# Kernel tuning notes

Measured on AMD Instinct MI355X. Metric: run time of the kernel, lower is better.

## Reference

```python
import jax, jax.numpy as jnp
import numpy as np
import math

H = 16  # n_head
DK = 64  # d_k = n_feat // n_head
BASE = 10000.0


def _rope_cos_sin(T, dk, dtype):
    inv_freq = 1.0 / (BASE ** (jnp.arange(0, dk, 2, dtype=jnp.float32) / dk))
    t = jnp.arange(T, dtype=jnp.float32)
    freqs = jnp.einsum('i,j->ij', t, inv_freq)          # [T, dk/2]
    emb = jnp.concatenate([freqs, freqs], axis=-1)       # [T, dk]
    return jnp.cos(emb).astype(dtype)[:, None, None, :], jnp.sin(emb).astype(dtype)[:, None, None, :]


def _rotate_half(x):
    x1, x2 = jnp.split(x, 2, axis=-1)
    return jnp.concatenate([-x2, x1], axis=-1)


def setup_inputs() -> dict:
    key = jax.random.key(0)
    ks = jax.random.split(key, 8)
    T, B, C = 2048, 2, 1024
    s = 0.02
    return {
        'query': jax.random.normal(ks[0], (T, B, C), jnp.float32),
        'key': jax.random.normal(ks[1], (T, B, C), jnp.float32),
        'value': jax.random.normal(ks[2], (T, B, C), jnp.float32),
        'Wq': jax.random.normal(ks[3], (C, C), jnp.float32) * s,
        'bq': jnp.zeros((C,), jnp.float32),
        'Wk': jax.random.normal(ks[4], (C, C), jnp.float32) * s,
        'bk': jnp.zeros((C,), jnp.float32),
        'Wv': jax.random.normal(ks[5], (C, C), jnp.float32) * s,
        'bv': jnp.zeros((C,), jnp.float32),
        'Wo': jax.random.normal(ks[6], (C, C), jnp.float32) * s,
        'bo': jnp.zeros((C,), jnp.float32),
    }


def reference(query, key, value, Wq, bq, Wk, bk, Wv, bv, Wo, bo):
    T, B, C = value.shape
    # --- RoPE applied to raw inputs (per the original module), before projections ---
    q = query.reshape(T, B, H, DK)
    k = key.reshape(T, B, H, DK)
    cos, sin = _rope_cos_sin(T, DK, q.dtype)  # [T,1,1,DK]
    q = q * cos + _rotate_half(q) * sin
    k = k * cos + _rotate_half(k) * sin
    q = q.reshape(T, B, C).transpose(1, 0, 2)   # [B,T,C]
    k = k.reshape(T, B, C).transpose(1, 0, 2)
    v = value.transpose(1, 0, 2)
    # --- QKV projections (torch Linear: x @ W.T + b) ---
    q = (jnp.einsum('btc,dc->btd', q, Wq) + bq).reshape(B, T, H, DK).transpose(0, 2, 1, 3)
    k = (jnp.einsum('btc,dc->btd', k, Wk) + bk).reshape(B, T, H, DK).transpose(0, 2, 1, 3)
    v = (jnp.einsum('btc,dc->btd', v, Wv) + bv).reshape(B, T, H, DK).transpose(0, 2, 1, 3)
    # --- scaled dot-product attention ---
    scores = jnp.einsum('bhqd,bhkd->bhqk', q, k) / math.sqrt(DK)
    attn = jax.nn.softmax(scores, axis=-1)
    x = jnp.einsum('bhqk,bhkd->bhqd', attn, v)        # [B,H,T,DK]
    x = x.transpose(0, 2, 1, 3).reshape(B, T, C)
    out = jnp.einsum('btc,dc->btd', x, Wo) + bo        # [B,T,C]
    return out.transpose(1, 0, 2)                      # [T,B,C]
```

## Files before the change

kernel.cpp:

```cpp
#include <hip/hip_runtime.h>
#include <hip/hip_bf16.h>
#include <math.h>

#define T_SEQ 2048
#define B_SZ 2
#define C_DIM 1024
#define H_HEADS 16
#define DKH 64
#define M_ROWS (T_SEQ * B_SZ)

#define QSCALE 0.1803368801111204f

typedef __attribute__((ext_vector_type(8))) short bf16x8;
typedef __attribute__((ext_vector_type(4))) float f32x4;
typedef unsigned short ushort_t;


__device__ __forceinline__ ushort_t f2bf(float f) {
    unsigned u = __float_as_uint(f);
    u += 0x7fffu + ((u >> 16) & 1u);
    return (ushort_t)(u >> 16);
}

__device__ __forceinline__ unsigned pack2bf(float a, float b) {
#if __has_builtin(__builtin_amdgcn_cvt_pk_bf16_f32)
    typedef __attribute__((ext_vector_type(2))) __bf16 bf16x2_t;
    union { bf16x2_t v; unsigned u; } cv;
    cv.v = __builtin_amdgcn_cvt_pk_bf16_f32(a, b);
    return cv.u;
#else
    return (unsigned)f2bf(a) | ((unsigned)f2bf(b) << 16);
#endif
}

__device__ __forceinline__ void async_copy16(const void* g, void* l) {
    __builtin_amdgcn_global_load_lds(
        (const __attribute__((address_space(1))) void*)g,
        (__attribute__((address_space(3))) void*)l, 16, 0, 0);
}

__global__ __launch_bounds__(256) void rope_cast_qk(
        const float* __restrict__ q, const float* __restrict__ k,
        ushort_t* __restrict__ qb, ushort_t* __restrict__ kb) {
    int idx  = blockIdx.x * 256 + threadIdx.x;
    int j    = idx & 31;
    int rest = idx >> 5;
    int h    = rest & (H_HEADS - 1);
    int tb   = rest >> 4;
    int t    = tb >> 1;
    float inv = exp2f(-(float)j * 0.41524101186092034f);
    float ang = (float)t * inv;
    float s, c;
    sincosf(ang, &s, &c);
    int base = tb * C_DIM + h * DKH + j;
    float q1 = q[base], q2 = q[base + 32];
    float k1 = k[base], k2 = k[base + 32];
    qb[base]      = f2bf(q1 * c - q2 * s);
    qb[base + 32] = f2bf(q2 * c + q1 * s);
    kb[base]      = f2bf(k1 * c - k2 * s);
    kb[base + 32] = f2bf(k2 * c + k1 * s);
}

__global__ __launch_bounds__(256) void cast_bf16_w4(
        const float* __restrict__ w0, const float* __restrict__ w1,
        const float* __restrict__ w2, const float* __restrict__ w3,
        ushort_t* __restrict__ o0, ushort_t* __restrict__ o1,
        ushort_t* __restrict__ o2, ushort_t* __restrict__ o3) {
    int which = blockIdx.y;
    const float* in = which == 0 ? w0 : which == 1 ? w1 : which == 2 ? w2 : w3;
    ushort_t*   out = which == 0 ? o0 : which == 1 ? o1 : which == 2 ? o2 : o3;
    int i = blockIdx.x * 256 + threadIdx.x;
    float4 v = reinterpret_cast<const float4*>(in)[i];
    ushort4 o;
    o.x = f2bf(v.x); o.y = f2bf(v.y); o.z = f2bf(v.z); o.w = f2bf(v.w);
    reinterpret_cast<ushort4*>(out)[i] = o;
}

__global__ __launch_bounds__(256) void cast_value_perm(
        const float* __restrict__ in, ushort_t* __restrict__ out) {
    int i   = blockIdx.x * 256 + threadIdx.x;
    int c4  = i & 255;
    int row = i >> 8;
    int b   = row >> 11, t = row & 2047;
    float4 v = reinterpret_cast<const float4*>(in)[(t * 2 + b) * 256 + c4];
    ushort4 o;
    o.x = f2bf(v.x); o.y = f2bf(v.y); o.z = f2bf(v.z); o.w = f2bf(v.w);
    reinterpret_cast<ushort4*>(out)[i] = o;
}

template <bool BF16_OUT, bool BIAS_ROW>
__global__ __launch_bounds__(512) void gemm_nt(
        const ushort_t* __restrict__ A, const ushort_t* __restrict__ W,
        const float* __restrict__ bias, void* __restrict__ Cout,
        int M, int N, int K, float scale) {
    __shared__ ushort_t As[2][128 * 64];
    __shared__ ushort_t Bs[2][64 * 64];
    const int tid  = threadIdx.x;
    const int lane = tid & 63;
    const int w    = tid >> 6;
    const int m16  = lane & 15, quad = lane >> 4;
    const int r8   = lane >> 3, c8 = lane & 7;
    const int clog = c8 ^ r8;
    const int rowBase = blockIdx.y * 128;
    const int colBase = blockIdx.x * 64;

    f32x4 acc[4];
#pragma unroll
    for (int j = 0; j < 4; j++) acc[j] = (f32x4){0.f, 0.f, 0.f, 0.f};

    auto stage = [&](int buf, int kt) {
#pragma unroll
        for (int i = 0; i < 2; ++i) {
            int R = w * 16 + i * 8;
            async_copy16(A + (size_t)(rowBase + R + r8) * K + kt + clog * 8,
                         &As[buf][R * 64]);
        }
        {
            int R = w * 8;
            async_copy16(W + (size_t)(colBase + R + r8) * K + kt + clog * 8,
                         &Bs[buf][R * 64]);
        }
    };

    stage(0, 0);
    int cur = 0;
    for (int kt = 0; kt < K; kt += 64, cur ^= 1) {
        if (kt + 64 < K) {
            stage(cur ^ 1, kt + 64);
            asm volatile("s_waitcnt vmcnt(3)" ::: "memory");
        } else {
            asm volatile("s_waitcnt vmcnt(0)" ::: "memory");
        }
        __builtin_amdgcn_s_barrier();
        __builtin_amdgcn_sched_barrier(0);
        const ushort_t* Asc = As[cur];
        const ushort_t* Bsc = Bs[cur];
#pragma unroll
        for (int ks = 0; ks < 2; ++ks) {
            int lc = ks * 4 + quad;
            bf16x8 af;
            {
                int R = w * 16 + m16;
                af = *reinterpret_cast<const bf16x8*>(
                    &Asc[R * 64 + ((lc ^ (R & 7)) << 3)]);
            }
            bf16x8 bfr[4];
#pragma unroll
            for (int ni = 0; ni < 4; ni++) {
                int R = ni * 16 + m16;
                bfr[ni] = *reinterpret_cast<const bf16x8*>(
                    &Bsc[R * 64 + ((lc ^ (R & 7)) << 3)]);
            }
#pragma unroll
            for (int ni = 0; ni < 4; ni++)
                acc[ni] = __builtin_amdgcn_mfma_f32_16x16x32_bf16(
                    af, bfr[ni], acc[ni], 0, 0, 0);
        }
        __builtin_amdgcn_s_barrier();
    }
#pragma unroll
    for (int ni = 0; ni < 4; ni++)
#pragma unroll
        for (int r = 0; r < 4; r++) {
            int row = rowBase + w * 16 + quad * 4 + r;
            int col = colBase + ni * 16 + m16;
            float v = (acc[ni][r] + (BIAS_ROW ? bias[row] : bias[col])) * scale;
            if (BF16_OUT)
                ((ushort_t*)Cout)[(size_t)row * N + col] = f2bf(v);
            else
                ((float*)Cout)[(size_t)row * N + col] = v;
        }
}

__global__ __launch_bounds__(256) void attn(
        const ushort_t* __restrict__ Qp, const ushort_t* __restrict__ Kp,
        const ushort_t* __restrict__ VTg, ushort_t* __restrict__ X) {
    __shared__ char smem[40960];
    ushort_t* Qt = (ushort_t*)smem;
    char*  KtC   = smem + 8192;
    char*  VTC   = smem + 24576;
    float* exch  = (float*)(smem + 8192);
    float* lbuf  = (float*)smem;

    const int tid  = threadIdx.x;
    const int lane = tid & 63;
    const int w    = tid >> 6;
    const int m16  = lane & 15, quad = lane >> 4;
    const int r8   = lane >> 3, c8 = lane & 7;
    const int clog = c8 ^ r8;

    const int lid   = blockIdx.x + blockIdx.y * 32;
    const int jj    = lid >> 3;
    const int pair  = (lid & 7) * 4 + (jj >> 5);
    const int qBase = (jj & 31) * 64;
    const int b = pair >> 4, h = pair & 15;

    const int ofA = m16 * 128 + ((quad ^ (m16 & 7)) << 4);
    const int ofB = m16 * 128 + (((4 + quad) ^ (m16 & 7)) << 4);
    const int sw4 = (m16 >> 1) & 3;
    const int fro = m16 * 64 + ((quad ^ sw4) << 4);
    int pw0[2];
#pragma unroll
    for (int kt_i = 0; kt_i < 2; kt_i++)
        pw0[kt_i] = m16 * 64 + (((kt_i * 2 + (quad >> 1)) ^ sw4) << 4) + (quad & 1) * 8;
    char* PwC = KtC + w * 4096;

    const int vlc = (lane & 3) ^ ((lane >> 3) & 3);

#pragma unroll
    for (int i = 0; i < 2; ++i) {
        int R = w * 16 + i * 8;
        async_copy16(Qp + (size_t)((qBase + R + r8) * 2 + b) * C_DIM + h * DKH + clog * 8,
                     &Qt[R * 64]);
    }
    __syncthreads();
    bf16x8 aq[4][2];
#pragma unroll
    for (int ni = 0; ni < 4; ni++) {
        aq[ni][0] = *reinterpret_cast<const bf16x8*>((const char*)Qt + ni * 2048 + ofA);
        aq[ni][1] = *reinterpret_cast<const bf16x8*>((const char*)Qt + ni * 2048 + ofB);
    }
    asm volatile("s_waitcnt lgkmcnt(0)" ::: "memory");
    __syncthreads();

    float lrun[4] = {0.f, 0.f, 0.f, 0.f};
    f32x4 o[4][4];
#pragma unroll
    for (int mi = 0; mi < 4; mi++)
#pragma unroll
        for (int ni = 0; ni < 4; ni++) o[mi][ni] = (f32x4){0.f, 0.f, 0.f, 0.f};

    auto stageKV = [&](int kt) {
#pragma unroll
        for (int i = 0; i < 4; ++i) {
            int key = kt + w * 32 + i * 8 + r8;
            async_copy16(Kp + (size_t)(key * 2 + b) * C_DIM + h * DKH + clog * 8,
                         KtC + w * 4096 + i * 1024);
        }
#pragma unroll
        for (int i = 0; i < 4; ++i) {
            int dkr = i * 16 + (lane >> 2);
            async_copy16(VTg + (size_t)(h * DKH + dkr) * M_ROWS + b * T_SEQ + kt + w * 32 + vlc * 8,
                         VTC + w * 4096 + i * 1024);
        }
    };

    stageKV(0);
    for (int kt = 0; kt < T_SEQ; kt += 128) {
        asm volatile("s_waitcnt vmcnt(4)" ::: "memory");
        __builtin_amdgcn_sched_barrier(0);

        f32x4 s[2][4];
#pragma unroll
        for (int kt_i = 0; kt_i < 2; kt_i++) {
#pragma unroll
            for (int ni = 0; ni < 4; ni++) s[kt_i][ni] = (f32x4){0.f, 0.f, 0.f, 0.f};
            bf16x8 kf0 = *reinterpret_cast<const bf16x8*>(KtC + w * 4096 + kt_i * 2048 + ofA);
            bf16x8 kf1 = *reinterpret_cast<const bf16x8*>(KtC + w * 4096 + kt_i * 2048 + ofB);
#pragma unroll
            for (int ni = 0; ni < 4; ni++) {
                s[kt_i][ni] = __builtin_amdgcn_mfma_f32_16x16x32_bf16(kf0, aq[ni][0], s[kt_i][ni], 0, 0, 0);
                s[kt_i][ni] = __builtin_amdgcn_mfma_f32_16x16x32_bf16(kf1, aq[ni][1], s[kt_i][ni], 0, 0, 0);
            }
        }

#pragma unroll
        for (int kt_i = 0; kt_i < 2; kt_i++)
#pragma unroll
            for (int ni = 0; ni < 4; ni++) {
                float p0 = __builtin_amdgcn_exp2f(s[kt_i][ni][0]);
                float p1 = __builtin_amdgcn_exp2f(s[kt_i][ni][1]);
                float p2 = __builtin_amdgcn_exp2f(s[kt_i][ni][2]);
                float p3 = __builtin_amdgcn_exp2f(s[kt_i][ni][3]);
                lrun[ni] += (p0 + p1) + (p2 + p3);
                uint2 pv;
                pv.x = pack2bf(p0, p1);
                pv.y = pack2bf(p2, p3);
                *reinterpret_cast<uint2*>(PwC + ni * 1024 + pw0[kt_i]) = pv;
            }
        asm volatile("s_waitcnt lgkmcnt(0)" ::: "memory");

        bf16x8 pf[4];
#pragma unroll
        for (int ni = 0; ni < 4; ni++)
            pf[ni] = *reinterpret_cast<const bf16x8*>(PwC + ni * 1024 + fro);
        asm volatile("s_waitcnt vmcnt(0)" ::: "memory");
        __builtin_amdgcn_sched_barrier(0);
        bf16x8 vfr[4];
#pragma unroll
        for (int mi = 0; mi < 4; mi++)
            vfr[mi] = *reinterpret_cast<const bf16x8*>(VTC + w * 4096 + mi * 1024 + fro);
        asm volatile("s_waitcnt lgkmcnt(0)" ::: "memory");
        __builtin_amdgcn_sched_barrier(0);
        if (kt + 128 < T_SEQ) stageKV(kt + 128);
        __builtin_amdgcn_sched_barrier(0);

#pragma unroll
        for (int mi = 0; mi < 4; mi++)
#pragma unroll
            for (int ni = 0; ni < 4; ni++)
                o[mi][ni] = __builtin_amdgcn_mfma_f32_16x16x32_bf16(vfr[mi], pf[ni], o[mi][ni], 0, 0, 0);
    }

#pragma unroll
    for (int ni = 0; ni < 4; ni++) {
        lrun[ni] += __shfl_xor(lrun[ni], 16);
        lrun[ni] += __shfl_xor(lrun[ni], 32);
    }
    float lv = quad == 0 ? lrun[0] : quad == 1 ? lrun[1] : quad == 2 ? lrun[2] : lrun[3];
    lbuf[w * 64 + quad * 16 + m16] = lv;

    __syncthreads();

#pragma unroll
    for (int rnd = 0; rnd < 2; rnd++) {
        if (rnd) __syncthreads();
#pragma unroll
        for (int t2 = 0; t2 < 2; t2++) {
            int mi = 2 * rnd + t2;
#pragma unroll
            for (int ni = 0; ni < 4; ni++) {
                int q = ni * 16 + m16;
                int cw = t2 * 4 + quad;
                *reinterpret_cast<f32x4*>(
                    &exch[w * 2048 + q * 32 + ((cw ^ (q & 7)) << 2)]) = o[mi][ni];
            }
        }
        __syncthreads();
        int q = tid >> 2;
        float lsum = lbuf[q] + lbuf[64 + q] + lbuf[128 + q] + lbuf[192 + q];
        float invl = 1.0f / lsum;
#pragma unroll
        for (int half = 0; half < 2; half++) {
            int c = (tid & 3) + 4 * half;
            int off = q * 32 + (((c ^ (q & 7))) << 2);
            f32x4 v = *reinterpret_cast<const f32x4*>(&exch[off]);
            f32x4 v1 = *reinterpret_cast<const f32x4*>(&exch[2048 + off]);
            f32x4 v2 = *reinterpret_cast<const f32x4*>(&exch[4096 + off]);
            f32x4 v3 = *reinterpret_cast<const f32x4*>(&exch[6144 + off]);
            v = v + v1 + v2 + v3;
            uint2 pk;
            pk.x = pack2bf(v[0] * invl, v[1] * invl);
            pk.y = pack2bf(v[2] * invl, v[3] * invl);
            int t = qBase + q;
            *reinterpret_cast<uint2*>(
                &X[(size_t)(t * 2 + b) * C_DIM + h * DKH + rnd * 32 + c * 4]) = pk;
        }
    }
}

extern "C" void kernel_launch(void* const* d_in, const int* in_sizes, int n_in,
                              void* d_out, int out_size, void* d_ws, size_t ws_size,
                              hipStream_t stream) {
    const float* query = (const float*)d_in[0];
    const float* key   = (const float*)d_in[1];
    const float* value = (const float*)d_in[2];
    const float* Wq = (const float*)d_in[3];
    const float* bq = (const float*)d_in[4];
    const float* Wk = (const float*)d_in[5];
    const float* bk = (const float*)d_in[6];
    const float* Wv = (const float*)d_in[7];
    const float* bv = (const float*)d_in[8];
    const float* Wo = (const float*)d_in[9];
    const float* bo = (const float*)d_in[10];
    float* out = (float*)d_out;

    ushort_t* qb  = (ushort_t*)d_ws;
    ushort_t* kb  = qb  + (size_t)M_ROWS * C_DIM;
    ushort_t* vb2 = kb  + (size_t)M_ROWS * C_DIM;
    ushort_t* Wqb = vb2 + (size_t)M_ROWS * C_DIM;
    ushort_t* Wkb = Wqb + (size_t)C_DIM * C_DIM;
    ushort_t* Wvb = Wkb + (size_t)C_DIM * C_DIM;
    ushort_t* Wob = Wvb + (size_t)C_DIM * C_DIM;
    ushort_t* Qp  = Wob + (size_t)C_DIM * C_DIM;
    ushort_t* Kp  = Qp  + (size_t)M_ROWS * C_DIM;
    ushort_t* VTg = Kp  + (size_t)M_ROWS * C_DIM;
    ushort_t* Xb  = VTg + (size_t)M_ROWS * C_DIM;

    rope_cast_qk<<<(T_SEQ * B_SZ * H_HEADS * 32) / 256, 256, 0, stream>>>(query, key, qb, kb);
    cast_value_perm<<<(M_ROWS * C_DIM / 4) / 256, 256, 0, stream>>>(value, vb2);
    dim3 cg((C_DIM * C_DIM / 4) / 256, 4);
    cast_bf16_w4<<<cg, 256, 0, stream>>>(Wq, Wk, Wv, Wo, Wqb, Wkb, Wvb, Wob);

    dim3 gg(C_DIM / 64, M_ROWS / 128);
    gemm_nt<true, false><<<gg, 512, 0, stream>>>(qb, Wqb, bq, Qp, M_ROWS, C_DIM, C_DIM, QSCALE);
    gemm_nt<true, false><<<gg, 512, 0, stream>>>(kb, Wkb, bk, Kp, M_ROWS, C_DIM, C_DIM, 1.0f);
    dim3 gv(M_ROWS / 64, C_DIM / 128);
    gemm_nt<true, true><<<gv, 512, 0, stream>>>(Wvb, vb2, bv, VTg, C_DIM, M_ROWS, C_DIM, 1.0f);

    attn<<<dim3(T_SEQ / 64, B_SZ * H_HEADS), 256, 0, stream>>>(Qp, Kp, VTg, Xb);

    gemm_nt<false, false><<<gg, 512, 0, stream>>>(Xb, Wob, bo, (void*)out, M_ROWS, C_DIM, C_DIM, 1.0f);
}
```

Measured before the change: 240.2 us.

## Halve GEMM block threads with two row-tiles per wave; simplify attention vmcnt waits

The GEMM keeps its 128x64 block tile but now runs 4 waves instead of 8. Each wave computes a 32x64 sub-tile (2x4 MFMA accumulators), so each B fragment read from LDS is reused across two A fragments. The intent is less LDS read traffic and barrier cost per MFMA, at the price of more registers per thread and fewer waves to hide latency. The attention kernel now waits for all outstanding global loads at the top of each iteration, which removes the separate later wait but reduces overlap of the K/V prefetch.

```diff
diff --git a/kernel.cpp b/kernel.cpp
--- a/kernel.cpp
+++ b/kernel.cpp
@@ -89,7 +89,7 @@
 }
 
 template <bool BF16_OUT, bool BIAS_ROW>
-__global__ __launch_bounds__(512) void gemm_nt(
+__global__ __launch_bounds__(256) void gemm_nt(
         const ushort_t* __restrict__ A, const ushort_t* __restrict__ W,
         const float* __restrict__ bias, void* __restrict__ Cout,
         int M, int N, int K, float scale) {
@@ -104,19 +104,22 @@
     const int rowBase = blockIdx.y * 128;
     const int colBase = blockIdx.x * 64;
 
-    f32x4 acc[4];
-#pragma unroll
-    for (int j = 0; j < 4; j++) acc[j] = (f32x4){0.f, 0.f, 0.f, 0.f};
+    f32x4 acc[2][4];
+#pragma unroll
+    for (int mi = 0; mi < 2; mi++)
+#pragma unroll
+        for (int ni = 0; ni < 4; ni++) acc[mi][ni] = (f32x4){0.f, 0.f, 0.f, 0.f};
 
     auto stage = [&](int buf, int kt) {
+#pragma unroll
+        for (int i = 0; i < 4; ++i) {
+            int R = w * 32 + i * 8;
+            async_copy16(A + (size_t)(rowBase + R + r8) * K + kt + clog * 8,
+                         &As[buf][R * 64]);
+        }
 #pragma unroll
         for (int i = 0; i < 2; ++i) {
             int R = w * 16 + i * 8;
-            async_copy16(A + (size_t)(rowBase + R + r8) * K + kt + clog * 8,
-                         &As[buf][R * 64]);
-        }
-        {
-            int R = w * 8;
             async_copy16(W + (size_t)(colBase + R + r8) * K + kt + clog * 8,
                          &Bs[buf][R * 64]);
         }
@@ -127,7 +130,7 @@
     for (int kt = 0; kt < K; kt += 64, cur ^= 1) {
         if (kt + 64 < K) {
             stage(cur ^ 1, kt + 64);
-            asm volatile("s_waitcnt vmcnt(3)" ::: "memory");
+            asm volatile("s_waitcnt vmcnt(6)" ::: "memory");
         } else {
             asm volatile("s_waitcnt vmcnt(0)" ::: "memory");
         }
@@ -138,10 +141,11 @@
 #pragma unroll
         for (int ks = 0; ks < 2; ++ks) {
             int lc = ks * 4 + quad;
-            bf16x8 af;
-            {
-                int R = w * 16 + m16;
-                af = *reinterpret_cast<const bf16x8*>(
+            bf16x8 af[2];
+#pragma unroll
+            for (int mi = 0; mi < 2; mi++) {
+                int R = w * 32 + mi * 16 + m16;
+                af[mi] = *reinterpret_cast<const bf16x8*>(
                     &Asc[R * 64 + ((lc ^ (R & 7)) << 3)]);
             }
             bf16x8 bfr[4];
@@ -152,24 +156,28 @@
                     &Bsc[R * 64 + ((lc ^ (R & 7)) << 3)]);
             }
 #pragma unroll
-            for (int ni = 0; ni < 4; ni++)
-                acc[ni] = __builtin_amdgcn_mfma_f32_16x16x32_bf16(
-                    af, bfr[ni], acc[ni], 0, 0, 0);
+            for (int mi = 0; mi < 2; mi++)
+#pragma unroll
+                for (int ni = 0; ni < 4; ni++)
+                    acc[mi][ni] = __builtin_amdgcn_mfma_f32_16x16x32_bf16(
+                        af[mi], bfr[ni], acc[mi][ni], 0, 0, 0);
         }
         __builtin_amdgcn_s_barrier();
     }
 #pragma unroll
-    for (int ni = 0; ni < 4; ni++)
-#pragma unroll
-        for (int r = 0; r < 4; r++) {
-            int row = rowBase + w * 16 + quad * 4 + r;
-            int col = colBase + ni * 16 + m16;
-            float v = (acc[ni][r] + (BIAS_ROW ? bias[row] : bias[col])) * scale;
-            if (BF16_OUT)
-                ((ushort_t*)Cout)[(size_t)row * N + col] = f2bf(v);
-            else
-                ((float*)Cout)[(size_t)row * N + col] = v;
-        }
+    for (int mi = 0; mi < 2; mi++)
+#pragma unroll
+        for (int ni = 0; ni < 4; ni++)
+#pragma unroll
+            for (int r = 0; r < 4; r++) {
+                int row = rowBase + w * 32 + mi * 16 + quad * 4 + r;
+                int col = colBase + ni * 16 + m16;
+                float v = (acc[mi][ni][r] + (BIAS_ROW ? bias[row] : bias[col])) * scale;
+                if (BF16_OUT)
+                    ((ushort_t*)Cout)[(size_t)row * N + col] = f2bf(v);
+                else
+                    ((float*)Cout)[(size_t)row * N + col] = v;
+            }
 }
 
 __global__ __launch_bounds__(256) void attn(
@@ -247,7 +255,7 @@
 
     stageKV(0);
     for (int kt = 0; kt < T_SEQ; kt += 128) {
-        asm volatile("s_waitcnt vmcnt(4)" ::: "memory");
+        asm volatile("s_waitcnt vmcnt(0)" ::: "memory");
         __builtin_amdgcn_sched_barrier(0);
 
         f32x4 s[2][4];
@@ -284,8 +292,6 @@
 #pragma unroll
         for (int ni = 0; ni < 4; ni++)
             pf[ni] = *reinterpret_cast<const bf16x8*>(PwC + ni * 1024 + fro);
-        asm volatile("s_waitcnt vmcnt(0)" ::: "memory");
-        __builtin_amdgcn_sched_barrier(0);
         bf16x8 vfr[4];
 #pragma unroll
         for (int mi = 0; mi < 4; mi++)
@@ -383,12 +389,12 @@
     cast_bf16_w4<<<cg, 256, 0, stream>>>(Wq, Wk, Wv, Wo, Wqb, Wkb, Wvb, Wob);
 
     dim3 gg(C_DIM / 64, M_ROWS / 128);
-    gemm_nt<true, false><<<gg, 512, 0, stream>>>(qb, Wqb, bq, Qp, M_ROWS, C_DIM, C_DIM, QSCALE);
-    gemm_nt<true, false><<<gg, 512, 0, stream>>>(kb, Wkb, bk, Kp, M_ROWS, C_DIM, C_DIM, 1.0f);
+    gemm_nt<true, false><<<gg, 256, 0, stream>>>(qb, Wqb, bq, Qp, M_ROWS, C_DIM, C_DIM, QSCALE);
+    gemm_nt<true, false><<<gg, 256, 0, stream>>>(kb, Wkb, bk, Kp, M_ROWS, C_DIM, C_DIM, 1.0f);
     dim3 gv(M_ROWS / 64, C_DIM / 128);
-    gemm_nt<true, true><<<gv, 512, 0, stream>>>(Wvb, vb2, bv, VTg, C_DIM, M_ROWS, C_DIM, 1.0f);
+    gemm_nt<true, true><<<gv, 256, 0, stream>>>(Wvb, vb2, bv, VTg, C_DIM, M_ROWS, C_DIM, 1.0f);
 
     attn<<<dim3(T_SEQ / 64, B_SZ * H_HEADS), 256, 0, stream>>>(Qp, Kp, VTg, Xb);
 
-    gemm_nt<false, false><<<gg, 512, 0, stream>>>(Xb, Wob, bo, (void*)out, M_ROWS, C_DIM, C_DIM, 1.0f);
-}
+    gemm_nt<false, false><<<gg, 256, 0, stream>>>(Xb, Wob, bo, (void*)out, M_ROWS, C_DIM, C_DIM, 1.0f);
+}
```

Result: no change. 240.7 us (+0.2%).
